# Kernel optimization log

Measured on AMD Instinct MI355X. Metric: run time of the kernel, lower is better.

## Reference

```python
import jax, jax.numpy as jnp
import numpy as np

B, S, D, H = 2, 2048, 1024, 16
DK = D // H
SCALE = DK ** 0.5


def setup_inputs() -> dict:
    key = jax.random.key(0)
    ks = jax.random.split(key, 5)
    std = 1.0 / np.sqrt(D)
    return {
        "x": jax.random.normal(ks[0], (B, S, D), dtype=jnp.float32),
        "Wq": jax.random.normal(ks[1], (D, D), dtype=jnp.float32) * std,
        "Wk": jax.random.normal(ks[2], (D, D), dtype=jnp.float32) * std,
        "Wv": jax.random.normal(ks[3], (D, D), dtype=jnp.float32) * std,
        "Wo": jax.random.normal(ks[4], (D, D), dtype=jnp.float32) * std,
    }


def _split_heads(t):
    # [B, S, D] -> [B, H, S, DK]
    b, s, d = t.shape
    return t.reshape(b, s, H, DK).transpose(0, 2, 1, 3)


def reference(x, Wq, Wk, Wv, Wo):
    b, s, d = x.shape
    q = _split_heads(x @ Wq)
    k = _split_heads(x @ Wk)
    v = _split_heads(x @ Wv)
    # scores: [B, H, S, S]
    score = jnp.einsum("bhqd,bhkd->bhqk", q, k)
    causal = jnp.tril(jnp.ones((s, s), dtype=bool))[None, None]
    score = jnp.where(causal, score, -jnp.inf)
    attn = jax.nn.softmax(score / SCALE, axis=-1)
    out = jnp.einsum("bhqk,bhkd->bhqd", attn, v)
    out = out.transpose(0, 2, 1, 3).reshape(b, s, d)
    return out @ Wo
```

## Files before the change

kernel.cpp:

```cpp
#include <hip/hip_runtime.h>
#include <hip/hip_bf16.h>

typedef __bf16 bf16;
typedef __bf16 bf16x4 __attribute__((ext_vector_type(4)));
typedef __bf16 bf16x8 __attribute__((ext_vector_type(8)));
typedef float f32x4 __attribute__((ext_vector_type(4)));

#define MFMA16(a, b, c) __builtin_amdgcn_mfma_f32_16x16x32_bf16((a), (b), (c), 0, 0, 0)

__device__ __forceinline__ void async16(const void* g, void* l) {
  typedef const unsigned int __attribute__((address_space(1))) * GP;
  typedef unsigned int __attribute__((address_space(3))) * LP;
  __builtin_amdgcn_global_load_lds((GP)g, (LP)l, 16, 0, 0);
}

__global__ __launch_bounds__(256) void prep(
    const float* __restrict__ w0, const float* __restrict__ w1,
    const float* __restrict__ w2, const float* __restrict__ w3,
    const float* __restrict__ x, bf16* __restrict__ wtOut,
    bf16* __restrict__ xOut) {
  const int t = threadIdx.x;
  if (blockIdx.z == 4) {
    size_t base = ((size_t)(blockIdx.y * 16 + blockIdx.x)) * 16384;
#pragma unroll
    for (int p = 0; p < 16; ++p) {
      size_t i = base + (size_t)(p * 256 + t) * 4;
      f32x4 v = *(const f32x4*)&x[i];
      bf16 o[4];
#pragma unroll
      for (int j = 0; j < 4; ++j) o[j] = (bf16)v[j];
      *(ulong1*)&xOut[i] = *(ulong1*)o;
    }
    return;
  }
  __shared__ __align__(16) float tile[64][68];
  const float* src = (blockIdx.z == 0) ? w0 : (blockIdx.z == 1) ? w1
                   : (blockIdx.z == 2) ? w2 : w3;
  bf16* dst = wtOut + (size_t)blockIdx.z * (1024u * 1024u);
  const int bx = blockIdx.x, by = blockIdx.y;
#pragma unroll
  for (int p = 0; p < 4; ++p) {
    int idx = t + p * 256;
    int r = idx >> 4, c4 = idx & 15;
    *(f32x4*)&tile[r][c4 * 4] =
        *(const f32x4*)&src[(size_t)(by * 64 + r) * 1024 + bx * 64 + c4 * 4];
  }
  __syncthreads();
#pragma unroll
  for (int p = 0; p < 2; ++p) {
    int idx = t + p * 256;
    int rn = idx >> 3, c8 = idx & 7;
    bf16x8 v;
#pragma unroll
    for (int i = 0; i < 8; ++i) v[i] = (bf16)tile[c8 * 8 + i][rn];
    *(bf16x8*)&dst[(size_t)(bx * 64 + rn) * 1024 + by * 64 + c8 * 8] = v;
  }
}

template <typename OutT, int NI>
__global__ __launch_bounds__(256, 4) void gemm_bt(
    const bf16* __restrict__ A, const bf16* __restrict__ Bt,
    OutT* __restrict__ C, int btStrideZ, int cStrideZ, float scaleZ0,
    bf16* __restrict__ vtOut) {
  constexpr int XT = 1024 / (NI * 32);
  const int bid = blockIdx.x;
  const int rr = bid & 7, tt = bid >> 3;
  const int xb = tt % XT, yb = (tt / XT) * 8 + rr;
  const int zi = blockIdx.y;

  const int tid = threadIdx.x;
  const int wave = tid >> 6, lane = tid & 63;
  const int quad = lane >> 4, l16 = lane & 15;
  const int wm = wave >> 1, wn = wave & 1;
  const int m0 = yb * 128, n0 = xb * (NI * 32);
  const bf16* Bz = Bt + (size_t)zi * (size_t)btStrideZ;
  OutT* Cz = C + (size_t)zi * (size_t)cStrideZ;
  const float sc = (zi == 0) ? scaleZ0 : 1.0f;

  __shared__ __align__(16) bf16 lsA[2][128 * 32];
  __shared__ __align__(16) bf16 lsB[2][NI * 32 * 32];

  const int lrow = lane >> 2;
  const int cgX = (lane & 3) ^ ((lrow >> 1) & 3);
  const int fR = (l16 >> 1) & 3;

  f32x4 acc[4][NI];
#pragma unroll
  for (int i = 0; i < 4; ++i)
#pragma unroll
    for (int j = 0; j < NI; ++j) acc[i][j] = (f32x4){0.f, 0.f, 0.f, 0.f};

#pragma unroll
  for (int c = 0; c < 2; ++c) {
    int chunk = wave * 2 + c;
    int row = chunk * 16 + lrow;
    async16(&A[(size_t)(m0 + row) * 1024 + cgX * 8], &lsA[0][chunk * 512]);
  }
#pragma unroll
  for (int c = 0; c < NI / 2; ++c) {
    int chunk = wave * (NI / 2) + c;
    int row = chunk * 16 + lrow;
    async16(&Bz[(size_t)(n0 + row) * 1024 + cgX * 8], &lsB[0][chunk * 512]);
  }
  __syncthreads();

  for (int it = 0; it < 32; ++it) {
    const int cur = it & 1;
    if (it < 31) {
      int k0n = (it + 1) * 32;
#pragma unroll
      for (int c = 0; c < 2; ++c) {
        int chunk = wave * 2 + c;
        int row = chunk * 16 + lrow;
        async16(&A[(size_t)(m0 + row) * 1024 + k0n + cgX * 8],
                &lsA[cur ^ 1][chunk * 512]);
      }
#pragma unroll
      for (int c = 0; c < NI / 2; ++c) {
        int chunk = wave * (NI / 2) + c;
        int row = chunk * 16 + lrow;
        async16(&Bz[(size_t)(n0 + row) * 1024 + k0n + cgX * 8],
                &lsB[cur ^ 1][chunk * 512]);
      }
    }

    bf16x8 af[4], bfr[NI];
#pragma unroll
    for (int i = 0; i < 4; ++i) {
      int ra = wm * 64 + i * 16 + l16;
      af[i] = *(const bf16x8*)&lsA[cur][ra * 32 + ((quad ^ fR) * 8)];
    }
#pragma unroll
    for (int ni = 0; ni < NI; ++ni) {
      int rb = wn * (NI * 16) + ni * 16 + l16;
      bfr[ni] = *(const bf16x8*)&lsB[cur][rb * 32 + ((quad ^ fR) * 8)];
    }
#pragma unroll
    for (int mi = 0; mi < 4; ++mi)
#pragma unroll
      for (int ni = 0; ni < NI; ++ni)
        acc[mi][ni] = MFMA16(af[mi], bfr[ni], acc[mi][ni]);

    __syncthreads();
  }

  if (zi == 2 && vtOut != nullptr) {
#pragma unroll
    for (int mi = 0; mi < 4; ++mi)
#pragma unroll
      for (int ni = 0; ni < NI; ++ni) {
        int col = n0 + wn * (NI * 16) + ni * 16 + l16;
        int hd = col >> 6, d = col & 63;
        int row = m0 + wm * 64 + mi * 16 + quad * 4;
        int b = row >> 11, s = row & 2047;
        int s32 = s & 31;
        int sp = (s & ~31) + ((s32 & 12) << 1) + ((s32 >> 4) << 2);
        bf16 o[4];
#pragma unroll
        for (int r = 0; r < 4; ++r) o[r] = (bf16)acc[mi][ni][r];
        *(ulong1*)&vtOut[((size_t)(b * 16 + hd) * 64 + d) * 2048 + sp] =
            *(ulong1*)o;
      }
  } else {
#pragma unroll
    for (int mi = 0; mi < 4; ++mi)
#pragma unroll
      for (int ni = 0; ni < NI; ++ni) {
        int col = n0 + wn * (NI * 16) + ni * 16 + l16;
#pragma unroll
        for (int r = 0; r < 4; ++r) {
          int row = m0 + wm * 64 + mi * 16 + quad * 4 + r;
          Cz[(size_t)row * 1024 + col] = (OutT)(acc[mi][ni][r] * sc);
        }
      }
  }
}

__global__ __launch_bounds__(512, 4) void attn_fwd(
    const bf16* __restrict__ Q, const bf16* __restrict__ K,
    const bf16* __restrict__ Vt, bf16* __restrict__ O) {
  const int bid = blockIdx.x;
  const int x = bid & 15, hb = bid >> 4;
  const int h = hb & 15, b = hb >> 4;
  const int qt = b ? (15 - x) : x;
  const int tid = threadIdx.x;
  const int wave = tid >> 6, lane = tid & 63;
  const int quad = lane >> 4, l16 = lane & 15;

  __shared__ __align__(16) bf16 SMEM[32768];
  bf16* Qs = &SMEM[16384];

  const size_t base = ((size_t)b * 2048) * 1024 + (size_t)h * 64;
  const bf16* Qb = Q + base;
  const bf16* Kb = K + base;
  const bf16* Vtb = Vt + ((size_t)(b * 16 + h)) * 64 * 2048;
  bf16* Ob = O + base;

  const int lrow = lane >> 3;
  const int cgX = (lane & 7) ^ lrow;

#pragma unroll
  for (int c = 0; c < 2; ++c) {
    int chunk = wave * 2 + c;
    int row = chunk * 8 + lrow;
    async16(&Qb[(size_t)(qt * 128 + row) * 1024 + cgX * 8], &Qs[chunk * 512]);
  }
  {
    int row = wave * 8 + lrow;
    async16(&Kb[(size_t)row * 1024 + cgX * 8], &SMEM[0 * 8192 + wave * 512]);
    async16(&Vtb[(size_t)row * 2048 + cgX * 8],
            &SMEM[0 * 8192 + 4096 + wave * 512]);
    async16(&Kb[(size_t)(64 + row) * 1024 + cgX * 8],
            &SMEM[1 * 8192 + wave * 512]);
    async16(&Vtb[(size_t)row * 2048 + 64 + cgX * 8],
            &SMEM[1 * 8192 + 4096 + wave * 512]);
  }
  __syncthreads();

  bf16x8 aq[2];
#pragma unroll
  for (int ks = 0; ks < 2; ++ks) {
    int row = wave * 16 + l16;
    aq[ks] = *(const bf16x8*)&Qs[row * 64 + (((ks * 4 + quad) ^ (l16 & 7)) * 8)];
  }
  __syncthreads();

  const float NEG_INF = -__builtin_inff();
  f32x4 lsv = (f32x4){0.f, 0.f, 0.f, 0.f};
  f32x4 Oacc[4];
#pragma unroll
  for (int nt = 0; nt < 4; ++nt) Oacc[nt] = (f32x4){0.f, 0.f, 0.f, 0.f};

  const int kt_end = 2 * qt + 1;
  const int ktd = 2 * qt + (wave >> 2);

  for (int ktp = 0; ktp <= kt_end; ktp += 2) {
    {
      int row = wave * 8 + lrow;
      if (ktp + 2 <= kt_end) {
        int s2 = (ktp + 2) & 3;
        async16(&Kb[(size_t)((ktp + 2) * 64 + row) * 1024 + cgX * 8],
                &SMEM[s2 * 8192 + wave * 512]);
        async16(&Vtb[(size_t)row * 2048 + (ktp + 2) * 64 + cgX * 8],
                &SMEM[s2 * 8192 + 4096 + wave * 512]);
      }
      if (ktp + 3 <= kt_end) {
        int s3 = (ktp + 3) & 3;
        async16(&Kb[(size_t)((ktp + 3) * 64 + row) * 1024 + cgX * 8],
                &SMEM[s3 * 8192 + wave * 512]);
        async16(&Vtb[(size_t)row * 2048 + (ktp + 3) * 64 + cgX * 8],
                &SMEM[s3 * 8192 + 4096 + wave * 512]);
      }
    }

#pragma unroll
    for (int sub = 0; sub < 2; ++sub) {
      const int kt = ktp + sub;
      const int ko = (kt & 3) * 8192;
      const int vo = ko + 4096;
      if (kt <= ktd) {
        f32x4 sv[4];
#pragma unroll
        for (int nt = 0; nt < 4; ++nt) {
          int row = nt * 16 + l16;
          bf16x8 bk0 = *(const bf16x8*)&SMEM[ko + row * 64 +
                                             ((quad ^ (l16 & 7)) * 8)];
          bf16x8 bk1 = *(const bf16x8*)&SMEM[ko + row * 64 +
                                             (((4 + quad) ^ (l16 & 7)) * 8)];
          sv[nt] = (f32x4){0.f, 0.f, 0.f, 0.f};
          sv[nt] = MFMA16(bk0, aq[0], sv[nt]);
          sv[nt] = MFMA16(bk1, aq[1], sv[nt]);
        }

        if (kt == ktd) {
          const int q_rel = wave * 16 + l16;
          const int cb = (kt - 2 * qt) * 64;
#pragma unroll
          for (int nt = 0; nt < 4; ++nt) {
            const int kb = cb + nt * 16 + quad * 4;
#pragma unroll
            for (int r = 0; r < 4; ++r)
              if (kb + r > q_rel) sv[nt][r] = NEG_INF;
          }
        }

#pragma unroll
        for (int nt = 0; nt < 4; ++nt) {
#pragma unroll
          for (int r = 0; r < 4; ++r) sv[nt][r] = exp2f(sv[nt][r]);
          lsv += sv[nt];
        }
        bf16x8 apf[2];
#pragma unroll
        for (int a = 0; a < 2; ++a) {
          bf16x4 c0 = __builtin_convertvector(sv[2 * a], bf16x4);
          bf16x4 c1 = __builtin_convertvector(sv[2 * a + 1], bf16x4);
#pragma unroll
          for (int i = 0; i < 4; ++i) {
            apf[a][i] = c0[i];
            apf[a][4 + i] = c1[i];
          }
        }

#pragma unroll
        for (int nt = 0; nt < 4; ++nt) {
          const int R = nt * 16 + l16;
#pragma unroll
          for (int a = 0; a < 2; ++a) {
            bf16x8 bvf = *(const bf16x8*)&SMEM[vo + R * 64 +
                                               (((a * 4 + quad) ^ (l16 & 7)) *
                                                8)];
            Oacc[nt] = MFMA16(apf[a], bvf, Oacc[nt]);
          }
        }
      }
    }

    __syncthreads();
  }

  float ls_acc = lsv[0] + lsv[1] + lsv[2] + lsv[3];
  ls_acc += __shfl_xor(ls_acc, 16, 64);
  ls_acc += __shfl_xor(ls_acc, 32, 64);
  float rl[4];
#pragma unroll
  for (int r = 0; r < 4; ++r) rl[r] = 1.f / __shfl(ls_acc, quad * 4 + r, 64);
#pragma unroll
  for (int nt = 0; nt < 4; ++nt)
#pragma unroll
    for (int r = 0; r < 4; ++r) {
      int row = qt * 128 + wave * 16 + quad * 4 + r;
      Ob[(size_t)row * 1024 + nt * 16 + l16] = (bf16)(Oacc[nt][r] * rl[r]);
    }
}

extern "C" void kernel_launch(void* const* d_in, const int* in_sizes, int n_in,
                              void* d_out, int out_size, void* d_ws,
                              size_t ws_size, hipStream_t stream) {
  (void)in_sizes; (void)n_in; (void)out_size; (void)ws_size;
  const float* x  = (const float*)d_in[0];
  const float* Wq = (const float*)d_in[1];
  const float* Wk = (const float*)d_in[2];
  const float* Wv = (const float*)d_in[3];
  const float* Wo = (const float*)d_in[4];
  float* out = (float*)d_out;

  bf16* ws = (bf16*)d_ws;
  const size_t WELEM = 1024u * 1024u;
  const size_t TELEM = 4096u * 1024u;
  bf16* wt  = ws;
  bf16* xbf = ws + 4 * WELEM;
  bf16* q   = xbf + TELEM;
  bf16* k   = q + TELEM;
  bf16* vt  = k + TELEM;
  bf16* ao  = vt + TELEM;

  const float QSCALE = 0.125f * 1.44269504088896340736f;

  prep<<<dim3(16, 16, 5), 256, 0, stream>>>(Wq, Wk, Wv, Wo, x, wt, xbf);
  gemm_bt<bf16, 4><<<dim3(256, 3), 256, 0, stream>>>(
      xbf, wt, q, (int)WELEM, (int)TELEM, QSCALE, vt);
  attn_fwd<<<dim3(512), 512, 0, stream>>>(q, k, vt, ao);
  gemm_bt<float, 2><<<dim3(512, 1), 256, 0, stream>>>(
      ao, wt + 3 * WELEM, out, 0, 0, 1.0f, nullptr);
}
```

Baseline: 168.1 us.

## Split key tiles across wave pairs, each wave handling 32 query rows

Each wave now owns 32 query rows (two 16-row groups) and handles only one of the two key tiles per loop iteration, chosen by wave parity, instead of 16 rows over both tiles. Every K and V fragment read from LDS now feeds two MFMAs, which halves LDS read traffic per MFMA. The partial O accumulators and row sums from the odd-parity wave are combined with the even wave's through shared memory at the end. This costs more registers per thread and adds an extra reduction pass and barrier before the output write.

```diff
diff --git a/kernel.cpp b/kernel.cpp
--- a/kernel.cpp
+++ b/kernel.cpp
@@ -186,6 +186,8 @@
   const int tid = threadIdx.x;
   const int wave = tid >> 6, lane = tid & 63;
   const int quad = lane >> 4, l16 = lane & 15;
+  const int wq = wave >> 1;
+  const int par = wave & 1;
 
   __shared__ __align__(16) bf16 SMEM[32768];
   bf16* Qs = &SMEM[16384];
@@ -217,24 +219,31 @@
   }
   __syncthreads();
 
-  bf16x8 aq[2];
-#pragma unroll
-  for (int ks = 0; ks < 2; ++ks) {
-    int row = wave * 16 + l16;
-    aq[ks] = *(const bf16x8*)&Qs[row * 64 + (((ks * 4 + quad) ^ (l16 & 7)) * 8)];
-  }
+  bf16x8 aq[2][2];
+#pragma unroll
+  for (int g = 0; g < 2; ++g)
+#pragma unroll
+    for (int ks = 0; ks < 2; ++ks) {
+      int row = wq * 32 + g * 16 + l16;
+      aq[g][ks] =
+          *(const bf16x8*)&Qs[row * 64 + (((ks * 4 + quad) ^ (l16 & 7)) * 8)];
+    }
   __syncthreads();
 
   const float NEG_INF = -__builtin_inff();
-  f32x4 lsv = (f32x4){0.f, 0.f, 0.f, 0.f};
-  f32x4 Oacc[4];
-#pragma unroll
-  for (int nt = 0; nt < 4; ++nt) Oacc[nt] = (f32x4){0.f, 0.f, 0.f, 0.f};
-
+  f32x4 lsv[2];
+  f32x4 Oacc[2][4];
+#pragma unroll
+  for (int g = 0; g < 2; ++g) {
+    lsv[g] = (f32x4){0.f, 0.f, 0.f, 0.f};
+#pragma unroll
+    for (int nt = 0; nt < 4; ++nt) Oacc[g][nt] = (f32x4){0.f, 0.f, 0.f, 0.f};
+  }
+
+  const int two_qt = 2 * qt;
   const int kt_end = 2 * qt + 1;
-  const int ktd = 2 * qt + (wave >> 2);
-
-  for (int ktp = 0; ktp <= kt_end; ktp += 2) {
+
+  for (int ktp = 0; ktp <= two_qt; ktp += 2) {
     {
       int row = wave * 8 + lrow;
       if (ktp + 2 <= kt_end) {
@@ -253,65 +262,76 @@
       }
     }
 
-#pragma unroll
-    for (int sub = 0; sub < 2; ++sub) {
-      const int kt = ktp + sub;
-      const int ko = (kt & 3) * 8192;
-      const int vo = ko + 4096;
-      if (kt <= ktd) {
-        f32x4 sv[4];
+    const int kt = ktp + par;
+    const int ko = (kt & 3) * 8192;
+    const int vo = ko + 4096;
+    const bool diag = (ktp == two_qt);
+    const bool active = !diag || (par == 0) || (wq >= 2);
+
+    if (active) {
+      f32x4 sv[2][4];
+#pragma unroll
+      for (int nt = 0; nt < 4; ++nt) {
+        int row = nt * 16 + l16;
+        bf16x8 bk0 =
+            *(const bf16x8*)&SMEM[ko + row * 64 + ((quad ^ (l16 & 7)) * 8)];
+        bf16x8 bk1 = *(const bf16x8*)&SMEM[ko + row * 64 +
+                                           (((4 + quad) ^ (l16 & 7)) * 8)];
+#pragma unroll
+        for (int g = 0; g < 2; ++g) {
+          f32x4 s = (f32x4){0.f, 0.f, 0.f, 0.f};
+          s = MFMA16(bk0, aq[g][0], s);
+          s = MFMA16(bk1, aq[g][1], s);
+          sv[g][nt] = s;
+        }
+      }
+
+      if (diag) {
+#pragma unroll
+        for (int g = 0; g < 2; ++g) {
+          const int q_rel = wq * 32 + g * 16 + l16;
+#pragma unroll
+          for (int nt = 0; nt < 4; ++nt) {
+            const int kb = par * 64 + nt * 16 + quad * 4;
+#pragma unroll
+            for (int r = 0; r < 4; ++r)
+              if (kb + r > q_rel) sv[g][nt][r] = NEG_INF;
+          }
+        }
+      }
+
+      bf16x8 apf[2][2];
+#pragma unroll
+      for (int g = 0; g < 2; ++g) {
 #pragma unroll
         for (int nt = 0; nt < 4; ++nt) {
-          int row = nt * 16 + l16;
-          bf16x8 bk0 = *(const bf16x8*)&SMEM[ko + row * 64 +
-                                             ((quad ^ (l16 & 7)) * 8)];
-          bf16x8 bk1 = *(const bf16x8*)&SMEM[ko + row * 64 +
-                                             (((4 + quad) ^ (l16 & 7)) * 8)];
-          sv[nt] = (f32x4){0.f, 0.f, 0.f, 0.f};
-          sv[nt] = MFMA16(bk0, aq[0], sv[nt]);
-          sv[nt] = MFMA16(bk1, aq[1], sv[nt]);
-        }
-
-        if (kt == ktd) {
-          const int q_rel = wave * 16 + l16;
-          const int cb = (kt - 2 * qt) * 64;
-#pragma unroll
-          for (int nt = 0; nt < 4; ++nt) {
-            const int kb = cb + nt * 16 + quad * 4;
-#pragma unroll
-            for (int r = 0; r < 4; ++r)
-              if (kb + r > q_rel) sv[nt][r] = NEG_INF;
+#pragma unroll
+          for (int r = 0; r < 4; ++r) sv[g][nt][r] = exp2f(sv[g][nt][r]);
+          lsv[g] += sv[g][nt];
+        }
+#pragma unroll
+        for (int a = 0; a < 2; ++a) {
+          bf16x4 c0 = __builtin_convertvector(sv[g][2 * a], bf16x4);
+          bf16x4 c1 = __builtin_convertvector(sv[g][2 * a + 1], bf16x4);
+#pragma unroll
+          for (int i = 0; i < 4; ++i) {
+            apf[g][a][i] = c0[i];
+            apf[g][a][4 + i] = c1[i];
           }
         }
-
-#pragma unroll
-        for (int nt = 0; nt < 4; ++nt) {
-#pragma unroll
-          for (int r = 0; r < 4; ++r) sv[nt][r] = exp2f(sv[nt][r]);
-          lsv += sv[nt];
-        }
-        bf16x8 apf[2];
+      }
+
+#pragma unroll
+      for (int nt = 0; nt < 4; ++nt) {
+        const int R = nt * 16 + l16;
 #pragma unroll
         for (int a = 0; a < 2; ++a) {
-          bf16x4 c0 = __builtin_convertvector(sv[2 * a], bf16x4);
-          bf16x4 c1 = __builtin_convertvector(sv[2 * a + 1], bf16x4);
-#pragma unroll
-          for (int i = 0; i < 4; ++i) {
-            apf[a][i] = c0[i];
-            apf[a][4 + i] = c1[i];
-          }
-        }
-
-#pragma unroll
-        for (int nt = 0; nt < 4; ++nt) {
-          const int R = nt * 16 + l16;
-#pragma unroll
-          for (int a = 0; a < 2; ++a) {
-            bf16x8 bvf = *(const bf16x8*)&SMEM[vo + R * 64 +
-                                               (((a * 4 + quad) ^ (l16 & 7)) *
-                                                8)];
-            Oacc[nt] = MFMA16(apf[a], bvf, Oacc[nt]);
-          }
+          bf16x8 bvf = *(const bf16x8*)&SMEM[vo + R * 64 +
+                                             (((a * 4 + quad) ^ (l16 & 7)) *
+                                              8)];
+#pragma unroll
+          for (int g = 0; g < 2; ++g)
+            Oacc[g][nt] = MFMA16(apf[g][a], bvf, Oacc[g][nt]);
         }
       }
     }
@@ -319,19 +339,52 @@
     __syncthreads();
   }
 
-  float ls_acc = lsv[0] + lsv[1] + lsv[2] + lsv[3];
-  ls_acc += __shfl_xor(ls_acc, 16, 64);
-  ls_acc += __shfl_xor(ls_acc, 32, 64);
-  float rl[4];
-#pragma unroll
-  for (int r = 0; r < 4; ++r) rl[r] = 1.f / __shfl(ls_acc, quad * 4 + r, 64);
-#pragma unroll
-  for (int nt = 0; nt < 4; ++nt)
-#pragma unroll
-    for (int r = 0; r < 4; ++r) {
-      int row = qt * 128 + wave * 16 + quad * 4 + r;
-      Ob[(size_t)row * 1024 + nt * 16 + l16] = (bf16)(Oacc[nt][r] * rl[r]);
-    }
+  float ls[2];
+#pragma unroll
+  for (int g = 0; g < 2; ++g) {
+    float a_ = lsv[g][0] + lsv[g][1] + lsv[g][2] + lsv[g][3];
+    a_ += __shfl_xor(a_, 16, 64);
+    a_ += __shfl_xor(a_, 32, 64);
+    ls[g] = a_;
+  }
+
+  float* F = (float*)SMEM;
+  const int roff = wq * 2176;
+  if (par == 1) {
+#pragma unroll
+    for (int g = 0; g < 2; ++g) {
+#pragma unroll
+      for (int nt = 0; nt < 4; ++nt)
+        *(f32x4*)&F[roff + (g * 4 + nt) * 256 + lane * 4] = Oacc[g][nt];
+      F[roff + 2048 + g * 64 + lane] = ls[g];
+    }
+  }
+  __syncthreads();
+  if (par == 0) {
+#pragma unroll
+    for (int g = 0; g < 2; ++g) {
+#pragma unroll
+      for (int nt = 0; nt < 4; ++nt)
+        Oacc[g][nt] += *(const f32x4*)&F[roff + (g * 4 + nt) * 256 + lane * 4];
+      ls[g] += F[roff + 2048 + g * 64 + lane];
+    }
+    float rl[2][4];
+#pragma unroll
+    for (int g = 0; g < 2; ++g)
+#pragma unroll
+      for (int r = 0; r < 4; ++r)
+        rl[g][r] = 1.f / __shfl(ls[g], quad * 4 + r, 64);
+#pragma unroll
+    for (int g = 0; g < 2; ++g)
+#pragma unroll
+      for (int nt = 0; nt < 4; ++nt)
+#pragma unroll
+        for (int r = 0; r < 4; ++r) {
+          int row = qt * 128 + wq * 32 + g * 16 + quad * 4 + r;
+          Ob[(size_t)row * 1024 + nt * 16 + l16] =
+              (bf16)(Oacc[g][nt][r] * rl[g][r]);
+        }
+  }
 }
 
 extern "C" void kernel_launch(void* const* d_in, const int* in_sizes, int n_in,
```

Result: no change. 169.5 us (+0.8%).
